# Kernel optimization log

Hardware: AMD Instinct MI355X
Metric: run time of the kernel (lower is better)

## Reference

```python
import jax, jax.numpy as jnp
import numpy as np

B, H, S, D = 1, 32, 2048, 128
SINK_LENGTH = 4   # prefill-start sink tokens excluded from quantization
N_OUTLIERS = 8    # outliers isolated per slice along the outlier dim
QMAX = 127.0      # int8 symmetric


def _isolate(x, dim, sink_len, r):
    """Zero sink tokens, extract top-|r| magnitude outliers along `dim`.
    Returns (dense_with_outliers_zeroed, sparse_values, sparse_indices)."""
    s_tok = x.shape[-2]
    sink_mask = (jnp.arange(s_tok) < sink_len)[:, None]          # [S,1] over (seq, head_dim)
    x_ns = jnp.where(sink_mask, jnp.zeros((), x.dtype), x)
    moved = jnp.moveaxis(x_ns, dim, -1)                          # outlier dim last
    lead, L = moved.shape[:-1], moved.shape[-1]
    flat = moved.reshape(-1, L)
    _, idx = jax.lax.top_k(jnp.abs(flat), r)                     # [N, r]
    rows = jnp.arange(flat.shape[0])[:, None]
    sp_val = flat[rows, idx]
    dense_flat = flat.at[rows, idx].set(0.0)
    dense = jnp.moveaxis(dense_flat.reshape(*lead, L), -1, dim)
    return dense, sp_val.reshape(*lead, r), idx.reshape(*lead, r).astype(jnp.int32)


def _quantize(x, absmax):
    scale = absmax / QMAX + 1e-8
    q = jnp.clip(jnp.round(x / scale), -QMAX, QMAX).astype(jnp.int8)
    return q, scale


def setup_inputs() -> dict:
    key = jax.random.key(0)
    kq, kk, kv = jax.random.split(key, 3)
    return {
        "q_tensor": jax.random.normal(kq, (B, H, S, D), dtype=jnp.float32),
        "k_tensor": jax.random.normal(kk, (B, H, S, D), dtype=jnp.float32),
        "v_tensor": jax.random.normal(kv, (B, H, S, D), dtype=jnp.float32),
    }


def reference(q_tensor, k_tensor, v_tensor):
    d = q_tensor.shape[-1]
    s = q_tensor.shape[-2]
    # --- causal attention over the current (prefill) chunk, empty cache ---
    scores = jnp.einsum("bhqd,bhkd->bhqk", q_tensor, k_tensor) / jnp.sqrt(jnp.asarray(d, q_tensor.dtype))
    causal = jnp.tril(jnp.ones((s, s), dtype=bool))
    scores = jnp.where(causal, scores, jnp.asarray(-1e30, scores.dtype))
    probs = jax.nn.softmax(scores, axis=-1)
    attn_out = jnp.einsum("bhqk,bhkd->bhqd", probs, v_tensor)
    # --- outlier isolation: K along token dim (-2), V along channel dim (-1) ---
    k_dense, k_sp_val, k_sp_idx = _isolate(k_tensor, -2, SINK_LENGTH, N_OUTLIERS)
    v_dense, v_sp_val, v_sp_idx = _isolate(v_tensor, -1, SINK_LENGTH, N_OUTLIERS)
    # --- stats: per-channel absmax for K, per-token absmax for V ---
    k_absmax = jnp.max(jnp.abs(k_dense), axis=-2, keepdims=True)  # [B,H,1,D]
    v_absmax = jnp.max(jnp.abs(v_dense), axis=-1, keepdims=True)  # [B,H,S,1]
    # --- int8 symmetric quantization of dense residual ---
    k_quant, k_scale = _quantize(k_dense, k_absmax)
    v_quant, v_scale = _quantize(v_dense, v_absmax)
    return (attn_out, k_quant, k_scale, k_sp_val, k_sp_idx,
            v_quant, v_scale, v_sp_val, v_sp_idx)
```

## Files before the change

### kernel.cpp

```cpp
#include <hip/hip_runtime.h>
#include <math.h>
#include <stdint.h>

#define H 32
#define S 2048
#define D 128
#define SINK 4
#define NOUT 8
#define QMAXF 127.0f

typedef unsigned short ushort_t;
typedef unsigned int uint_t;

#define OFF_ATTN   0u
#define OFF_KQUANT 8388608u
#define OFF_KSCALE 16777216u
#define OFF_KSPV   16781312u
#define OFF_KSPI   16814080u
#define OFF_VQUANT 16846848u
#define OFF_VSCALE 25235456u
#define OFF_VSPV   25300992u
#define OFF_VSPI   25825280u

typedef __attribute__((ext_vector_type(8))) short short8;
typedef __attribute__((ext_vector_type(4))) float f32x4;

__device__ inline unsigned long long wave_max_u64(unsigned long long key) {
#pragma unroll
    for (int off = 1; off < 64; off <<= 1) {
        unsigned lo = (unsigned)key, hi = (unsigned)(key >> 32);
        unsigned olo = __shfl_xor(lo, off);
        unsigned ohi = __shfl_xor(hi, off);
        unsigned long long o = ((unsigned long long)ohi << 32) | olo;
        if (o > key) key = o;
    }
    return key;
}

__device__ inline float wave_max_f32(float x) {
#pragma unroll
    for (int off = 1; off < 64; off <<= 1) x = fmaxf(x, __shfl_xor(x, off));
    return x;
}

__device__ inline ushort_t bf16rtn(float x) {
    uint_t u = __float_as_uint(x);
    return (ushort_t)((u + 0x7FFFu + ((u >> 16) & 1u)) >> 16);
}

__launch_bounds__(256, 2)
__global__ void attn_mfma(const float* __restrict__ Q, const float* __restrict__ K,
                          const float* __restrict__ V, float* __restrict__ O) {
    __shared__ __attribute__((aligned(16))) ushort_t Kh[64 * 128];
    __shared__ __attribute__((aligned(16))) ushort_t Vt[128 * 64];
    __shared__ __attribute__((aligned(16))) ushort_t Pl[4 * 16 * 64];

    const int h   = blockIdx.x;
    const int qb  = (int)gridDim.y - 1 - (int)blockIdx.y;
    const int tid = threadIdx.x;
    const int wid = tid >> 6, lane = tid & 63;
    const int g = lane >> 4, ql = lane & 15;

    const float* Qh = Q + (size_t)h * S * D;
    const float* Kg = K + (size_t)h * S * D;
    const float* Vg = V + (size_t)h * S * D;

    const int wq0 = qb * 64 + wid * 16;
    const int qg  = wq0 + ql;
    const float sc = 0.08838834764831845f;

    short8 qf[4];
#pragma unroll
    for (int dt = 0; dt < 4; ++dt) {
        const float* qp = Qh + (size_t)qg * D + dt * 32 + g * 8;
        float4 a = *(const float4*)qp;
        float4 b = *(const float4*)(qp + 4);
        float f[8] = {a.x, a.y, a.z, a.w, b.x, b.y, b.z, b.w};
        union { ushort_t us[8]; short8 v; } u;
#pragma unroll
        for (int j = 0; j < 8; ++j) u.us[j] = bf16rtn(f[j] * sc);
        qf[dt] = u.v;
    }

    f32x4 acc[8];
#pragma unroll
    for (int i = 0; i < 8; ++i) acc[i] = (f32x4){0.f, 0.f, 0.f, 0.f};
    float m = -1e30f, l = 0.f;

    const int ntiles = qb + 1;
    for (int t = 0; t < ntiles; ++t) {
        const int k0 = t * 64;
        __syncthreads();
#pragma unroll
        for (int i = 0; i < 4; ++i) {
            const int flat = i * 256 + tid;
            const int row = flat >> 4, c = flat & 15;
            const float* kp = Kg + (size_t)(k0 + row) * D + c * 8;
            float4 a = *(const float4*)kp;
            float4 b = *(const float4*)(kp + 4);
            float f[8] = {a.x, a.y, a.z, a.w, b.x, b.y, b.z, b.w};
            union { ushort_t us[8]; uint4 u4; } u;
#pragma unroll
            for (int j = 0; j < 8; ++j) u.us[j] = bf16rtn(f[j]);
            *(uint4*)&Kh[(row * 16 + (c ^ (row & 7))) * 8] = u.u4;
        }
        uint_t* VtU = (uint_t*)Vt;
#pragma unroll
        for (int uu = 0; uu < 2; ++uu) {
            const int p = (tid >> 4) + 16 * uu;
            const int c = tid & 15;
            const float* v0 = Vg + (size_t)(k0 + 2 * p) * D + c * 8;
            const float* v1 = v0 + D;
            float4 a0 = *(const float4*)v0, b0 = *(const float4*)(v0 + 4);
            float4 a1 = *(const float4*)v1, b1 = *(const float4*)(v1 + 4);
            float r0[8] = {a0.x, a0.y, a0.z, a0.w, b0.x, b0.y, b0.z, b0.w};
            float r1[8] = {a1.x, a1.y, a1.z, a1.w, b1.x, b1.y, b1.z, b1.w};
#pragma unroll
            for (int i = 0; i < 8; ++i) {
                const int dv = 8 * c + i;
                const int sv = (dv ^ (dv >> 3)) & 7;
                const uint_t pk = (uint_t)bf16rtn(r0[i]) | ((uint_t)bf16rtn(r1[i]) << 16);
                VtU[dv * 32 + (((p >> 2) ^ sv) << 2) + (p & 3)] = pk;
            }
        }
        __syncthreads();

        f32x4 sf[4];
#pragma unroll
        for (int st = 0; st < 4; ++st) {
            f32x4 a = (f32x4){0.f, 0.f, 0.f, 0.f};
#pragma unroll
            for (int dt = 0; dt < 4; ++dt) {
                const short8 kf =
                    *(const short8*)&Kh[((16 * st + ql) * 16 + ((g + 4 * dt) ^ (ql & 7))) * 8];
                a = __builtin_amdgcn_mfma_f32_16x16x32_bf16(kf, qf[dt], a, 0, 0, 0);
            }
            sf[st] = a;
        }
        if (k0 + 63 > wq0) {
#pragma unroll
            for (int st = 0; st < 4; ++st)
#pragma unroll
                for (int r = 0; r < 4; ++r) {
                    const int key = k0 + 16 * st + 4 * g + r;
                    if (key > qg) sf[st][r] = -1e30f;
                }
        }
        float tm = sf[0][0];
#pragma unroll
        for (int st = 0; st < 4; ++st)
#pragma unroll
            for (int r = 0; r < 4; ++r) tm = fmaxf(tm, sf[st][r]);
        tm = fmaxf(tm, __shfl_xor(tm, 16));
        tm = fmaxf(tm, __shfl_xor(tm, 32));
        if (__any(tm > m + 8.0f)) {
            const float mn = fmaxf(m, tm);
            const float f = __expf(m - mn);
            l *= f;
            float fr[4];
#pragma unroll
            for (int r = 0; r < 4; ++r) fr[r] = __shfl(f, g * 4 + r);
#pragma unroll
            for (int i = 0; i < 8; ++i)
#pragma unroll
                for (int r = 0; r < 4; ++r) acc[i][r] *= fr[r];
            m = mn;
        }
        float ts = 0.f;
        uint2* PlU = (uint2*)Pl;
#pragma unroll
        for (int st = 0; st < 4; ++st) {
            float p0 = __expf(sf[st][0] - m);
            float p1 = __expf(sf[st][1] - m);
            float p2 = __expf(sf[st][2] - m);
            float p3 = __expf(sf[st][3] - m);
            ts += (p0 + p1) + (p2 + p3);
            uint2 w;
            w.x = (uint_t)bf16rtn(p0) | ((uint_t)bf16rtn(p1) << 16);
            w.y = (uint_t)bf16rtn(p2) | ((uint_t)bf16rtn(p3) << 16);
            PlU[wid * 256 + ql * 16 + ((4 * st + g) ^ (2 * (ql & 7)))] = w;
        }
        ts += __shfl_xor(ts, 16);
        ts += __shfl_xor(ts, 32);
        l += ts;

        short8 pa[2];
#pragma unroll
        for (int ks = 0; ks < 2; ++ks)
            pa[ks] = *(const short8*)&Pl[(wid * 128 + ql * 8 + ((4 * ks + g) ^ (ql & 7))) * 8];
#pragma unroll
        for (int dvt = 0; dvt < 8; ++dvt) {
            const int dv = dvt * 16 + ql;
            const int sv = (dv ^ (dv >> 3)) & 7;
#pragma unroll
            for (int ks = 0; ks < 2; ++ks) {
                const short8 vf = *(const short8*)&Vt[(dv * 8 + ((g + 4 * ks) ^ sv)) * 8];
                acc[dvt] = __builtin_amdgcn_mfma_f32_16x16x32_bf16(pa[ks], vf, acc[dvt], 0, 0, 0);
            }
        }
    }

    float inv[4];
#pragma unroll
    for (int r = 0; r < 4; ++r) {
        const float lr = __shfl(l, g * 4 + r);
        inv[r] = 1.0f / lr;
    }
#pragma unroll
    for (int dvt = 0; dvt < 8; ++dvt)
#pragma unroll
        for (int r = 0; r < 4; ++r) {
            const int qq = wq0 + g * 4 + r;
            O[(size_t)(h * S + qq) * D + dvt * 16 + ql] = acc[dvt][r] * inv[r];
        }
}

__global__ void k_stats_kernel(const float* __restrict__ K, float* __restrict__ out) {
    const int w = threadIdx.x >> 6, lane = threadIdx.x & 63;
    const int col = blockIdx.x * 4 + w;
    const int h = col >> 7, d = col & 127;
    const float* base = K + (size_t)h * S * D + d;
    float v[32];
#pragma unroll
    for (int j = 0; j < 32; ++j) {
        const int s_idx = lane + 64 * j;
        const float x = base[(size_t)s_idx * D];
        v[j] = (s_idx < SINK) ? 0.f : x;
    }
    unsigned done = 0u;
    float spv[NOUT]; int spi[NOUT];
#pragma unroll
    for (int r = 0; r < NOUT; ++r) {
        unsigned best_a = 0u; unsigned best_i = 0x3FFFFFFFu; float best_v = 0.f;
#pragma unroll
        for (int j = 0; j < 32; ++j) {
            const unsigned a = __float_as_uint(v[j]) & 0x7fffffffu;
            const bool better = (!((done >> j) & 1u)) && (a > best_a);
            if (better) { best_a = a; best_i = (unsigned)(lane + 64 * j); best_v = v[j]; }
        }
        const unsigned long long key =
            ((unsigned long long)best_a << 32) | (unsigned)(~best_i);
        const unsigned long long wkey = wave_max_u64(key);
        const int widx = (int)(~(unsigned)wkey);
        const float wval = __shfl(best_v, widx & 63);
        spv[r] = wval; spi[r] = widx;
        if ((widx & 63) == lane) done |= 1u << (widx >> 6);
    }
    float am = 0.f;
#pragma unroll
    for (int j = 0; j < 32; ++j)
        if (!((done >> j) & 1u)) am = fmaxf(am, fabsf(v[j]));
    am = wave_max_f32(am);
    const float scl = am / QMAXF + 1e-8f;
    if (lane == 0) {
        out[OFF_KSCALE + col] = scl;
#pragma unroll
        for (int r = 0; r < NOUT; ++r) {
            out[OFF_KSPV + (size_t)col * 8 + r] = spv[r];
            out[OFF_KSPI + (size_t)col * 8 + r] = (float)spi[r];
        }
    }
}

__global__ void k_quant_kernel(const float* __restrict__ K, float* __restrict__ out) {
    const int gid = blockIdx.x * 256 + threadIdx.x;
    const int d = gid & 127;
    const int hs = gid >> 7;
    const int s_idx = hs & (S - 1);
    const int col = ((hs >> 11) << 7) | d;
    const float x = K[gid];
    const float scl = out[OFF_KSCALE + col];
    bool zero = (s_idx < SINK);
#pragma unroll
    for (int r = 0; r < NOUT; ++r)
        zero |= ((int)out[OFF_KSPI + (size_t)col * 8 + r] == s_idx);
    const float dense = zero ? 0.f : x;
    float q = rintf(dense / scl);
    q = fminf(fmaxf(q, -QMAXF), QMAXF);
    out[OFF_KQUANT + (size_t)gid] = q;
}

__global__ void v_kernel(const float* __restrict__ V, float* __restrict__ out) {
    const int w = threadIdx.x >> 6, lane = threadIdx.x & 63;
    const int row = blockIdx.x * 4 + w;
    const int s_idx = row & (S - 1);
    const float* base = V + (size_t)row * D;
    float2 vv = *reinterpret_cast<const float2*>(base + lane * 2);
    if (s_idx < SINK) { vv.x = 0.f; vv.y = 0.f; }
    const float v0 = vv.x, v1 = vv.y;
    const unsigned a0 = __float_as_uint(v0) & 0x7fffffffu;
    const unsigned a1 = __float_as_uint(v1) & 0x7fffffffu;
    const unsigned i0 = lane * 2, i1 = lane * 2 + 1;
    unsigned done = 0u;
    float spv[NOUT]; int spi[NOUT];
#pragma unroll
    for (int r = 0; r < NOUT; ++r) {
        const bool e0 = !(done & 1u), e1 = !(done & 2u);
        unsigned best_a, best_i; float best_v;
        if (e1 && (!e0 || a1 > a0)) { best_a = a1; best_i = i1; best_v = v1; }
        else if (e0)                { best_a = a0; best_i = i0; best_v = v0; }
        else                        { best_a = 0u; best_i = 0x3FFFFFFFu; best_v = 0.f; }
        const unsigned long long key =
            ((unsigned long long)best_a << 32) | (unsigned)(~best_i);
        const unsigned long long wkey = wave_max_u64(key);
        const int widx = (int)(~(unsigned)wkey);
        const float cand = (widx & 1) ? v1 : v0;
        const float wval = __shfl(cand, widx >> 1);
        spv[r] = wval; spi[r] = widx;
        if ((widx >> 1) == (int)lane) done |= (widx & 1) ? 2u : 1u;
    }
    float am = fmaxf((done & 1u) ? 0.f : __uint_as_float(a0),
                     (done & 2u) ? 0.f : __uint_as_float(a1));
    am = wave_max_f32(am);
    const float scl = am / QMAXF + 1e-8f;
    const float d0 = (done & 1u) ? 0.f : v0;
    const float d1 = (done & 2u) ? 0.f : v1;
    const float q0 = fminf(fmaxf(rintf(d0 / scl), -QMAXF), QMAXF);
    const float q1 = fminf(fmaxf(rintf(d1 / scl), -QMAXF), QMAXF);
    *reinterpret_cast<float2*>(out + OFF_VQUANT + (size_t)row * D + lane * 2) =
        make_float2(q0, q1);
    if (lane == 0) {
        out[OFF_VSCALE + row] = scl;
#pragma unroll
        for (int r = 0; r < NOUT; ++r) {
            out[OFF_VSPV + (size_t)row * 8 + r] = spv[r];
            out[OFF_VSPI + (size_t)row * 8 + r] = (float)spi[r];
        }
    }
}

extern "C" void kernel_launch(void* const* d_in, const int* in_sizes, int n_in,
                              void* d_out, int out_size, void* d_ws, size_t ws_size,
                              hipStream_t stream) {
    const float* Q = (const float*)d_in[0];
    const float* K = (const float*)d_in[1];
    const float* V = (const float*)d_in[2];
    float* out = (float*)d_out;

    attn_mfma<<<dim3(H, S / 64), 256, 0, stream>>>(Q, K, V, out + OFF_ATTN);
    k_stats_kernel<<<dim3((H * D) / 4), 256, 0, stream>>>(K, out);
    k_quant_kernel<<<dim3((H * S * D) / 256), 256, 0, stream>>>(K, out);
    v_kernel<<<dim3((H * S) / 4), 256, 0, stream>>>(V, out);
}
```

Measured before the change: 477.2 us.

## Stage K columns through swizzled LDS and pass outlier mask via bitmask

k_stats now loads an 8-column by 1024-row slab of K into shared memory with coalesced reads and an XOR swizzle, instead of each wave reading strided single columns. It also sets bits in a workspace bitmask for each outlier position. k_quant then reads one mask word per element rather than eight float index loads and compares. The cost is an extra memset of the workspace, atomics, and a 32 KB shared-memory tile per block, which may limit occupancy.

```diff
diff --git a/kernel.cpp b/kernel.cpp
--- a/kernel.cpp
+++ b/kernel.cpp
@@ -215,18 +215,38 @@
         }
 }
 
-__global__ void k_stats_kernel(const float* __restrict__ K, float* __restrict__ out) {
-    const int w = threadIdx.x >> 6, lane = threadIdx.x & 63;
-    const int col = blockIdx.x * 4 + w;
-    const int h = col >> 7, d = col & 127;
-    const float* base = K + (size_t)h * S * D + d;
+__launch_bounds__(512, 2)
+__global__ void k_stats_kernel(const float* __restrict__ K, float* __restrict__ out,
+                               uint_t* __restrict__ mask) {
+    __shared__ float Tile[8 * 1024];
+    const int tid = threadIdx.x;
+    const int w = tid >> 6, lane = tid & 63;
+    const int h  = blockIdx.x >> 4;
+    const int d0 = (blockIdx.x & 15) * 8;
+    const int d  = d0 + w;
+    const int col = h * 128 + d;
+    const float* Kh = K + (size_t)h * S * D + d0;
+
     float v[32];
 #pragma unroll
-    for (int j = 0; j < 32; ++j) {
-        const int s_idx = lane + 64 * j;
-        const float x = base[(size_t)s_idx * D];
-        v[j] = (s_idx < SINK) ? 0.f : x;
-    }
+    for (int ph = 0; ph < 2; ++ph) {
+        __syncthreads();
+#pragma unroll
+        for (int i = 0; i < 16; ++i) {
+            const int flat = i * 512 + tid;
+            const int s = flat >> 3, c = flat & 7;
+            Tile[c * 1024 + (s ^ (c << 2))] = Kh[(size_t)(ph * 1024 + s) * D + c];
+        }
+        __syncthreads();
+#pragma unroll
+        for (int j = 0; j < 16; ++j) {
+            const int sl = lane + 64 * j;
+            const float x = Tile[w * 1024 + (sl ^ (w << 2))];
+            const int s_idx = ph * 1024 + sl;
+            v[ph * 16 + j] = (s_idx < SINK) ? 0.f : x;
+        }
+    }
+
     unsigned done = 0u;
     float spv[NOUT]; int spi[NOUT];
 #pragma unroll
@@ -258,22 +278,24 @@
         for (int r = 0; r < NOUT; ++r) {
             out[OFF_KSPV + (size_t)col * 8 + r] = spv[r];
             out[OFF_KSPI + (size_t)col * 8 + r] = (float)spi[r];
-        }
-    }
-}
-
-__global__ void k_quant_kernel(const float* __restrict__ K, float* __restrict__ out) {
+            const int s = spi[r];
+            if (s >= 0 && s < S)
+                atomicOr(&mask[(((size_t)h * S + s) << 2) + (d >> 5)], 1u << (d & 31));
+        }
+    }
+}
+
+__global__ void k_quant_kernel(const float* __restrict__ K, float* __restrict__ out,
+                               const uint_t* __restrict__ mask) {
     const int gid = blockIdx.x * 256 + threadIdx.x;
     const int d = gid & 127;
     const int hs = gid >> 7;
     const int s_idx = hs & (S - 1);
     const int col = ((hs >> 11) << 7) | d;
     const float x = K[gid];
+    const uint_t wm = mask[((size_t)hs << 2) + (d >> 5)];
+    const bool zero = (s_idx < SINK) || ((wm >> (d & 31)) & 1u);
     const float scl = out[OFF_KSCALE + col];
-    bool zero = (s_idx < SINK);
-#pragma unroll
-    for (int r = 0; r < NOUT; ++r)
-        zero |= ((int)out[OFF_KSPI + (size_t)col * 8 + r] == s_idx);
     const float dense = zero ? 0.f : x;
     float q = rintf(dense / scl);
     q = fminf(fmaxf(q, -QMAXF), QMAXF);
@@ -336,9 +358,11 @@
     const float* K = (const float*)d_in[1];
     const float* V = (const float*)d_in[2];
     float* out = (float*)d_out;
-
+    uint_t* mask = (uint_t*)d_ws;
+
+    hipMemsetAsync(d_ws, 0, (size_t)H * S * D / 8, stream);
     attn_mfma<<<dim3(H, S / 64), 256, 0, stream>>>(Q, K, V, out + OFF_ATTN);
-    k_stats_kernel<<<dim3((H * D) / 4), 256, 0, stream>>>(K, out);
-    k_quant_kernel<<<dim3((H * S * D) / 256), 256, 0, stream>>>(K, out);
+    k_stats_kernel<<<dim3((H * D) / 8), 512, 0, stream>>>(K, out, mask);
+    k_quant_kernel<<<dim3((H * S * D) / 256), 256, 0, stream>>>(K, out, mask);
     v_kernel<<<dim3((H * S) / 4), 256, 0, stream>>>(V, out);
 }
```

After: 458.9 us. -3.8%, faster.
